# Kernel tuning notes

Measured on AMD Instinct MI355X. Metric: run time of the kernel, lower is better.

Reference implementation:

```python
import jax, jax.numpy as jnp
import numpy as np

B, C, H, W = 32, 512, 28, 28
NC, NM, K = 50, 4, 5          # num_classes, num_mixtures, num_clutter_models
OCC = 0.3                     # occ_likely[0]


def setup_inputs() -> dict:
    key = jax.random.key(0)
    k1, k2, k3 = jax.random.split(key, 3)
    x = jax.random.uniform(k1, (B, C, H, W), dtype=jnp.float32)
    mix_model = jax.random.uniform(k2, (NC * NM, C, H, W), dtype=jnp.float32)
    clutter_model = jax.random.uniform(k3, (K, C), dtype=jnp.float32)
    return {"x": x, "mix_model": mix_model, "clutter_model": clutter_model}


def _l1_normalize(a, axis):
    # torch: F.normalize(torch.clamp(a, 0, 1), p=1, dim=axis) with eps=1e-12
    a = jnp.clip(a, 0.0, 1.0)
    return a / jnp.maximum(jnp.sum(a, axis=axis, keepdims=True), 1e-12)


def reference(x, mix_model, clutter_model):
    # clutter: [K, C] -> L1-normalized over channels
    cl = _l1_normalize(clutter_model, axis=1)
    # background log-likelihood: (x.unsqueeze(1) * cl[:, :, None, None]).sum(2)
    bg = jnp.einsum('bchw,kc->bkhw', x, cl)            # [B, K, H, W]
    bg = jnp.log(bg * OCC + 1e-10)
    # mixture models: [M, C, H, W] -> L1-normalized over channels
    mm = _l1_normalize(mix_model, axis=1)
    # foreground log-likelihood: (x.unsqueeze(1) * mm).sum(2)
    fg = jnp.einsum('bchw,mchw->bmhw', x, mm)          # [B, M, H, W]
    fg = jnp.log(fg * (1.0 - OCC) + 1e-10)
    fg = fg.reshape(B, NC, NM, 1, H, W)
    # per-pixel occlusion max between foreground and background, sum over H, W
    per_model = jnp.maximum(fg, bg[:, None, None, :, :, :]).sum((-1, -2))  # [B, NC, NM, K]
    # max over clutter models, then over mixtures
    return per_model.max(axis=-1).max(axis=-1)          # [B, NC]
```

## Files before the change

### kernel.cpp

```cpp
#include <hip/hip_runtime.h>
#include <math.h>

#define Bc  32
#define Cc  512
#define HWc 784
#define Mc  200
#define Kc  5
#define NCc 50

#define PT    16
#define MT    32
#define CK    8
#define SPL   2
#define CSPL  256
#define NCH   32
#define NMT   7
#define NPT   49
#define CHF   4096

__device__ __forceinline__ void gl2lds16(const float* g, float* l) {
    __builtin_amdgcn_global_load_lds(
        (const __attribute__((address_space(1))) void*)g,
        (__attribute__((address_space(3))) void*)l, 16, 0, 0);
}

__global__ __launch_bounds__(256) void k_bg(const float* __restrict__ x,
                                            const float* __restrict__ clut,
                                            float* __restrict__ bgpart) {
    __shared__ float cl[Kc * Cc];
    __shared__ float csum[Kc];
    const int t = threadIdx.x;
    for (int i = t; i < Kc * Cc; i += 256) cl[i] = clut[i];
    __syncthreads();
    if (t < 160) {
        const int k = t >> 5, l = t & 31;
        float s = 0.0f;
        for (int c = l; c < Cc; c += 32) s += cl[k * Cc + c];
#pragma unroll
        for (int off = 16; off > 0; off >>= 1) s += __shfl_down(s, off, 32);
        if (l == 0) csum[k] = fmaxf(s, 1e-12f);
    }
    __syncthreads();

    const int b = blockIdx.x;
    const int z = blockIdx.z;
    const int hw = blockIdx.y * 256 + t;
    if (hw < HWc) {
        float acc[Kc] = {0.f, 0.f, 0.f, 0.f, 0.f};
        const int cbase = z * 128;
        const float* xb = x + ((size_t)b * Cc + cbase) * HWc + hw;
#pragma unroll 4
        for (int c = 0; c < 128; ++c) {
            const float xv = xb[c * HWc];
#pragma unroll
            for (int k = 0; k < Kc; ++k) acc[k] = fmaf(xv, cl[k * Cc + cbase + c], acc[k]);
        }
#pragma unroll
        for (int k = 0; k < Kc; ++k)
            bgpart[(((z * Bc + b) * Kc) + k) * HWc + hw] = acc[k] / csum[k];
    }
}

__global__ void k_bgsum(const float* __restrict__ bgpart, float* __restrict__ bgl) {
    const int i = blockIdx.x * 256 + threadIdx.x;
    const int N = Bc * Kc * HWc;
    if (i < N) {
        const float s = bgpart[i] + bgpart[i + N] + bgpart[i + 2 * N] + bgpart[i + 3 * N];
        bgl[i] = logf(0.3f * s + 1e-10f);
    }
}

__global__ __launch_bounds__(256) __attribute__((amdgpu_waves_per_eu(2, 2)))
void k_fg(const float* __restrict__ x, const float* __restrict__ mm,
          float* __restrict__ dotp, float* __restrict__ Sp) {
    __shared__ float ldsX[2][CHF];
    __shared__ float ldsM[2][CHF];

    const int t    = threadIdx.x;
    const int pixl = t & 3;
    const int mgr  = (t >> 2) & 3;
    const int bgp  = (t >> 4) & 3;
    const int pixh = t >> 6;
    const int pix  = pixl + 4 * pixh;

    const int mtile = blockIdx.x % NMT;
    const int ptile = (blockIdx.x / NMT) % NPT;
    const int split = blockIdx.x / (NMT * NPT);
    const int pix0  = ptile * PT;
    const int m0    = mtile * MT;
    const int c0    = split * CSPL;

    const int q4   = (t & 3) * 4;
    const int srow = (t >> 2) & 31;
    const int cx0  = t >> 7;
    const int mrow = (m0 + srow < Mc) ? (m0 + srow) : 0;
    const int ldst = 4 * t;

    int xg = (srow * Cc + c0 + cx0) * HWc + pix0 + q4;
    int mg = (mrow * Cc + c0 + cx0) * HWc + pix0 + q4;

    const int xoff = bgp * PT + pix;
    const int moff = mgr * PT + pix;

    float acc[8][8];
#pragma unroll
    for (int i = 0; i < 8; ++i)
#pragma unroll
        for (int j = 0; j < 8; ++j) acc[i][j] = 0.0f;
    float sacc[8] = {0.f, 0.f, 0.f, 0.f, 0.f, 0.f, 0.f, 0.f};

#pragma unroll
    for (int r = 0; r < 4; ++r) {
        gl2lds16(x + xg + 2 * r * HWc, &ldsX[0][ldst + 1024 * r]);
        gl2lds16(mm + mg + 2 * r * HWc, &ldsM[0][ldst + 1024 * r]);
    }
    xg += CK * HWc;
    mg += CK * HWc;

#pragma unroll 2
    for (int ch = 0; ch < NCH; ++ch) {
        __syncthreads();
        if (ch + 1 < NCH) {
            float* bx = &ldsX[(ch + 1) & 1][0];
            float* bm = &ldsM[(ch + 1) & 1][0];
#pragma unroll
            for (int r = 0; r < 4; ++r) {
                gl2lds16(x + xg + 2 * r * HWc, bx + ldst + 1024 * r);
                gl2lds16(mm + mg + 2 * r * HWc, bm + ldst + 1024 * r);
            }
            xg += CK * HWc;
            mg += CK * HWc;
        }
        const float* cbx = &ldsX[ch & 1][0];
        const float* cbm = &ldsM[ch & 1][0];
#pragma unroll
        for (int c = 0; c < CK; ++c) {
            float xv[8], mv[8];
#pragma unroll
            for (int i = 0; i < 8; ++i) xv[i] = cbx[c * 512 + 64 * i + xoff];
#pragma unroll
            for (int j = 0; j < 8; ++j) mv[j] = cbm[c * 512 + 64 * j + moff];
#pragma unroll
            for (int j = 0; j < 8; ++j) sacc[j] += mv[j];
#pragma unroll
            for (int i = 0; i < 8; ++i)
#pragma unroll
                for (int j = 0; j < 8; ++j)
                    acc[i][j] = fmaf(xv[i], mv[j], acc[i][j]);
        }
    }

    const int hw = pix0 + pix;
#pragma unroll
    for (int j = 0; j < 8; ++j) {
        const int m = m0 + mgr + 4 * j;
        if (m < Mc) {
            if (bgp == 0) Sp[(split * Mc + m) * HWc + hw] = sacc[j];
#pragma unroll
            for (int i = 0; i < 8; ++i) {
                const int b = bgp + 4 * i;
                dotp[((split * Mc + m) * Bc + b) * HWc + hw] = acc[i][j];
            }
        }
    }
}

__global__ __launch_bounds__(256) void k_red(const float* __restrict__ dotp,
                                             const float* __restrict__ Sp,
                                             const float* __restrict__ bgl,
                                             float* __restrict__ pm) {
    const int bm = blockIdx.x;
    const int b = bm / Mc;
    const int m = bm % Mc;
    const int t = threadIdx.x;
    const float* d0 = dotp + ((size_t)m * Bc + b) * HWc;
    const float* d1 = dotp + ((size_t)(Mc + m) * Bc + b) * HWc;
    const float* s0 = Sp + (size_t)m * HWc;
    const float* s1 = Sp + (size_t)(Mc + m) * HWc;
    const float* bgb = bgl + (size_t)b * Kc * HWc;

    float s[Kc] = {0.f, 0.f, 0.f, 0.f, 0.f};
    for (int hw = t; hw < HWc; hw += 256) {
        const float dot = d0[hw] + d1[hw];
        const float S   = s0[hw] + s1[hw];
        const float fgv = logf(0.7f * dot / fmaxf(S, 1e-12f) + 1e-10f);
#pragma unroll
        for (int k = 0; k < Kc; ++k) s[k] += fmaxf(fgv, bgb[k * HWc + hw]);
    }
#pragma unroll
    for (int off = 32; off > 0; off >>= 1) {
#pragma unroll
        for (int k = 0; k < Kc; ++k) s[k] += __shfl_down(s[k], off, 64);
    }
    __shared__ float red[4][Kc];
    const int wv = t >> 6, ln = t & 63;
    if (ln == 0) {
#pragma unroll
        for (int k = 0; k < Kc; ++k) red[wv][k] = s[k];
    }
    __syncthreads();
    if (t == 0) {
        float best = -INFINITY;
#pragma unroll
        for (int k = 0; k < Kc; ++k)
            best = fmaxf(best, red[0][k] + red[1][k] + red[2][k] + red[3][k]);
        pm[bm] = best;
    }
}

__global__ void k_out(const float* __restrict__ pm, float* __restrict__ out) {
    const int i = blockIdx.x * 256 + threadIdx.x;
    if (i < Bc * NCc) {
        const int b = i / NCc, nc = i % NCc;
        const float* p = pm + (size_t)b * Mc + nc * 4;
        out[i] = fmaxf(fmaxf(p[0], p[1]), fmaxf(p[2], p[3]));
    }
}

extern "C" void kernel_launch(void* const* d_in, const int* in_sizes, int n_in,
                              void* d_out, int out_size, void* d_ws, size_t ws_size,
                              hipStream_t stream) {
    const float* x    = (const float*)d_in[0];
    const float* mixm = (const float*)d_in[1];
    const float* clut = (const float*)d_in[2];
    float* out = (float*)d_out;

    float* dotp   = (float*)d_ws;
    float* Sp     = dotp + (size_t)SPL * Mc * Bc * HWc;
    float* bgpart = Sp + (size_t)SPL * Mc * HWc;
    float* bgl    = bgpart + (size_t)4 * Bc * Kc * HWc;
    float* pm     = bgl + (size_t)Bc * Kc * HWc;

    k_bg   <<<dim3(Bc, 4, 4), 256, 0, stream>>>(x, clut, bgpart);
    k_bgsum<<<dim3((Bc * Kc * HWc + 255) / 256), 256, 0, stream>>>(bgpart, bgl);
    k_fg   <<<dim3(NMT * NPT * SPL), 256, 0, stream>>>(x, mixm, dotp, Sp);
    k_red  <<<dim3(Bc * Mc), 256, 0, stream>>>(dotp, Sp, bgl, pm);
    k_out  <<<dim3(7), 256, 0, stream>>>(pm, out);
}
```

Measured before the change: 606.4 us.

## Compute foreground dot products with bf16 MFMA and fuse normalization and log

The fp32 FMA outer-product kernel is replaced by one that converts x and mixture tiles to bf16 in LDS and uses 16x16x32 bf16 MFMA instructions. A ones-vector MFMA produces the channel sums. The channel split is dropped, so the L1 normalization and log are applied directly in the epilogue and the reduce kernel reads a single fg array. This cuts FMA work and intermediate traffic, but bf16 rounding lowers precision and loads are now synchronous register-staged rather than async double-buffered.

```diff
diff --git a/kernel.cpp b/kernel.cpp
--- a/kernel.cpp
+++ b/kernel.cpp
@@ -8,20 +8,29 @@
 #define Kc  5
 #define NCc 50
 
-#define PT    16
-#define MT    32
-#define CK    8
-#define SPL   2
-#define CSPL  256
-#define NCH   32
-#define NMT   7
-#define NPT   49
-#define CHF   4096
-
-__device__ __forceinline__ void gl2lds16(const float* g, float* l) {
-    __builtin_amdgcn_global_load_lds(
-        (const __attribute__((address_space(1))) void*)g,
-        (__attribute__((address_space(3))) void*)l, 16, 0, 0);
+#define PTm   16
+#define MTm   16
+#define NMB   13
+#define NPB   49
+#define CKm   32
+#define NCHm  16
+#define RSTR  18
+#define XPL   (32*RSTR)
+#define MPL   (16*RSTR)
+#define MMBASE (16*XPL)
+#define LDSDW (16*XPL + 16*MPL)
+
+typedef short s8v __attribute__((ext_vector_type(8)));
+typedef float f4v __attribute__((ext_vector_type(4)));
+
+union F8 { uint2 u2[2]; s8v h; };
+
+__device__ __forceinline__ unsigned f2b(float f) {
+    union { float f; unsigned u; } v; v.f = f;
+    return (v.u + 0x7FFFu + ((v.u >> 16) & 1u)) >> 16;
+}
+__device__ __forceinline__ unsigned pk(float lo, float hi) {
+    return f2b(lo) | (f2b(hi) << 16);
 }
 
 __global__ __launch_bounds__(256) void k_bg(const float* __restrict__ x,
@@ -72,120 +81,143 @@
 
 __global__ __launch_bounds__(256) __attribute__((amdgpu_waves_per_eu(2, 2)))
 void k_fg(const float* __restrict__ x, const float* __restrict__ mm,
-          float* __restrict__ dotp, float* __restrict__ Sp) {
-    __shared__ float ldsX[2][CHF];
-    __shared__ float ldsM[2][CHF];
-
-    const int t    = threadIdx.x;
-    const int pixl = t & 3;
-    const int mgr  = (t >> 2) & 3;
-    const int bgp  = (t >> 4) & 3;
-    const int pixh = t >> 6;
-    const int pix  = pixl + 4 * pixh;
-
-    const int mtile = blockIdx.x % NMT;
-    const int ptile = (blockIdx.x / NMT) % NPT;
-    const int split = blockIdx.x / (NMT * NPT);
-    const int pix0  = ptile * PT;
-    const int m0    = mtile * MT;
-    const int c0    = split * CSPL;
-
-    const int q4   = (t & 3) * 4;
-    const int srow = (t >> 2) & 31;
-    const int cx0  = t >> 7;
-    const int mrow = (m0 + srow < Mc) ? (m0 + srow) : 0;
-    const int ldst = 4 * t;
-
-    int xg = (srow * Cc + c0 + cx0) * HWc + pix0 + q4;
-    int mg = (mrow * Cc + c0 + cx0) * HWc + pix0 + q4;
-
-    const int xoff = bgp * PT + pix;
-    const int moff = mgr * PT + pix;
-
-    float acc[8][8];
-#pragma unroll
-    for (int i = 0; i < 8; ++i)
-#pragma unroll
-        for (int j = 0; j < 8; ++j) acc[i][j] = 0.0f;
-    float sacc[8] = {0.f, 0.f, 0.f, 0.f, 0.f, 0.f, 0.f, 0.f};
-
-#pragma unroll
-    for (int r = 0; r < 4; ++r) {
-        gl2lds16(x + xg + 2 * r * HWc, &ldsX[0][ldst + 1024 * r]);
-        gl2lds16(mm + mg + 2 * r * HWc, &ldsM[0][ldst + 1024 * r]);
-    }
-    xg += CK * HWc;
-    mg += CK * HWc;
-
-#pragma unroll 2
-    for (int ch = 0; ch < NCH; ++ch) {
+          float* __restrict__ fg) {
+    __shared__ unsigned lds[LDSDW];
+
+    const int t = threadIdx.x;
+    const int mblk = blockIdx.x % NMB;
+    const int pix0 = (blockIdx.x / NMB) * PTm;
+
+    int xoff[4], xl[4];
+#pragma unroll
+    for (int g = 0; g < 4; ++g) {
+        const int G = t + 256 * g;
+        const int q = G & 3, b = (G >> 2) & 31, cg = G >> 7;
+        xoff[g] = (b * Cc + cg * 4) * HWc + pix0 + 4 * q;
+        xl[g]   = 4 * q * XPL + b * RSTR + cg * 2;
+    }
+    int moff[2], ml[2];
+    float mzero[2];
+#pragma unroll
+    for (int g = 0; g < 2; ++g) {
+        const int G = t + 256 * g;
+        const int q = G & 3, mr = (G >> 2) & 15, cg = (G >> 6) & 7;
+        const int mrow = mblk * MTm + mr;
+        mzero[g] = (mrow < Mc) ? 1.0f : 0.0f;
+        const int mc = (mrow < Mc) ? mrow : (Mc - 1);
+        moff[g] = (mc * Cc + cg * 4) * HWc + pix0 + 4 * q;
+        ml[g]   = MMBASE + 4 * q * MPL + mr * RSTR + cg * 2;
+    }
+
+    const int lane = t & 63;
+    const int w    = t >> 6;
+    const int row18q = (lane & 15) * RSTR + (lane >> 4) * 4;
+
+    f4v accD[4][2], accS[4];
+#pragma unroll
+    for (int p = 0; p < 4; ++p) {
+        accS[p] = (f4v)0.0f;
+#pragma unroll
+        for (int bt = 0; bt < 2; ++bt) accD[p][bt] = (f4v)0.0f;
+    }
+    const s8v ones = {0x3F80, 0x3F80, 0x3F80, 0x3F80, 0x3F80, 0x3F80, 0x3F80, 0x3F80};
+
+#pragma unroll 1
+    for (int ch = 0; ch < NCHm; ++ch) {
         __syncthreads();
-        if (ch + 1 < NCH) {
-            float* bx = &ldsX[(ch + 1) & 1][0];
-            float* bm = &ldsM[(ch + 1) & 1][0];
-#pragma unroll
-            for (int r = 0; r < 4; ++r) {
-                gl2lds16(x + xg + 2 * r * HWc, bx + ldst + 1024 * r);
-                gl2lds16(mm + mg + 2 * r * HWc, bm + ldst + 1024 * r);
-            }
-            xg += CK * HWc;
-            mg += CK * HWc;
-        }
-        const float* cbx = &ldsX[ch & 1][0];
-        const float* cbm = &ldsM[ch & 1][0];
-#pragma unroll
-        for (int c = 0; c < CK; ++c) {
-            float xv[8], mv[8];
-#pragma unroll
-            for (int i = 0; i < 8; ++i) xv[i] = cbx[c * 512 + 64 * i + xoff];
-#pragma unroll
-            for (int j = 0; j < 8; ++j) mv[j] = cbm[c * 512 + 64 * j + moff];
-#pragma unroll
-            for (int j = 0; j < 8; ++j) sacc[j] += mv[j];
-#pragma unroll
-            for (int i = 0; i < 8; ++i)
-#pragma unroll
-                for (int j = 0; j < 8; ++j)
-                    acc[i][j] = fmaf(xv[i], mv[j], acc[i][j]);
-        }
-    }
-
-    const int hw = pix0 + pix;
-#pragma unroll
-    for (int j = 0; j < 8; ++j) {
-        const int m = m0 + mgr + 4 * j;
-        if (m < Mc) {
-            if (bgp == 0) Sp[(split * Mc + m) * HWc + hw] = sacc[j];
-#pragma unroll
-            for (int i = 0; i < 8; ++i) {
-                const int b = bgp + 4 * i;
-                dotp[((split * Mc + m) * Bc + b) * HWc + hw] = acc[i][j];
-            }
-        }
-    }
-}
-
-__global__ __launch_bounds__(256) void k_red(const float* __restrict__ dotp,
-                                             const float* __restrict__ Sp,
+        float4 LX[4][4], LM[2][4];
+#pragma unroll
+        for (int g = 0; g < 4; ++g)
+#pragma unroll
+            for (int cc = 0; cc < 4; ++cc)
+                LX[g][cc] = *(const float4*)(x + xoff[g] + cc * HWc);
+#pragma unroll
+        for (int g = 0; g < 2; ++g)
+#pragma unroll
+            for (int cc = 0; cc < 4; ++cc)
+                LM[g][cc] = *(const float4*)(mm + moff[g] + cc * HWc);
+#pragma unroll
+        for (int g = 0; g < 4; ++g) xoff[g] += CKm * HWc;
+#pragma unroll
+        for (int g = 0; g < 2; ++g) moff[g] += CKm * HWc;
+
+#pragma unroll
+        for (int g = 0; g < 4; ++g) {
+            const float* f0 = (const float*)&LX[g][0];
+            const float* f1 = (const float*)&LX[g][1];
+            const float* f2 = (const float*)&LX[g][2];
+            const float* f3 = (const float*)&LX[g][3];
+#pragma unroll
+            for (int p = 0; p < 4; ++p)
+                *(uint2*)&lds[xl[g] + p * XPL] =
+                    make_uint2(pk(f0[p], f1[p]), pk(f2[p], f3[p]));
+        }
+#pragma unroll
+        for (int g = 0; g < 2; ++g) {
+            const float z = mzero[g];
+            const float* f0 = (const float*)&LM[g][0];
+            const float* f1 = (const float*)&LM[g][1];
+            const float* f2 = (const float*)&LM[g][2];
+            const float* f3 = (const float*)&LM[g][3];
+#pragma unroll
+            for (int p = 0; p < 4; ++p)
+                *(uint2*)&lds[ml[g] + p * MPL] =
+                    make_uint2(pk(f0[p] * z, f1[p] * z), pk(f2[p] * z, f3[p] * z));
+        }
+        __syncthreads();
+
+#pragma unroll
+        for (int p = 0; p < 4; ++p) {
+            const int pixg = w * 4 + p;
+            const unsigned* Xp = &lds[pixg * XPL + row18q];
+            const unsigned* Mp = &lds[MMBASE + pixg * MPL + row18q];
+            F8 a0, a1, bf;
+            a0.u2[0] = *(const uint2*)(Xp);
+            a0.u2[1] = *(const uint2*)(Xp + 2);
+            a1.u2[0] = *(const uint2*)(Xp + 16 * RSTR);
+            a1.u2[1] = *(const uint2*)(Xp + 16 * RSTR + 2);
+            bf.u2[0] = *(const uint2*)(Mp);
+            bf.u2[1] = *(const uint2*)(Mp + 2);
+            accD[p][0] = __builtin_amdgcn_mfma_f32_16x16x32_bf16(a0.h, bf.h, accD[p][0], 0, 0, 0);
+            accD[p][1] = __builtin_amdgcn_mfma_f32_16x16x32_bf16(a1.h, bf.h, accD[p][1], 0, 0, 0);
+            accS[p]    = __builtin_amdgcn_mfma_f32_16x16x32_bf16(ones, bf.h, accS[p],    0, 0, 0);
+        }
+    }
+
+    const int m = mblk * MTm + (lane & 15);
+    if (m < Mc) {
+        const int quad = lane >> 4;
+#pragma unroll
+        for (int p = 0; p < 4; ++p) {
+            const int hw = pix0 + w * 4 + p;
+            const float scale = 0.7f / fmaxf(accS[p][0], 1e-12f);
+#pragma unroll
+            for (int bt = 0; bt < 2; ++bt)
+#pragma unroll
+                for (int r = 0; r < 4; ++r) {
+                    const int b = bt * 16 + quad * 4 + r;
+                    fg[((size_t)m * Bc + b) * HWc + hw] =
+                        logf(accD[p][bt][r] * scale + 1e-10f);
+                }
+        }
+    }
+}
+
+__global__ __launch_bounds__(256) void k_red(const float* __restrict__ fg,
                                              const float* __restrict__ bgl,
                                              float* __restrict__ pm) {
     const int bm = blockIdx.x;
     const int b = bm / Mc;
     const int m = bm % Mc;
     const int t = threadIdx.x;
-    const float* d0 = dotp + ((size_t)m * Bc + b) * HWc;
-    const float* d1 = dotp + ((size_t)(Mc + m) * Bc + b) * HWc;
-    const float* s0 = Sp + (size_t)m * HWc;
-    const float* s1 = Sp + (size_t)(Mc + m) * HWc;
+    const float* fgp = fg + ((size_t)m * Bc + b) * HWc;
     const float* bgb = bgl + (size_t)b * Kc * HWc;
 
     float s[Kc] = {0.f, 0.f, 0.f, 0.f, 0.f};
     for (int hw = t; hw < HWc; hw += 256) {
-        const float dot = d0[hw] + d1[hw];
-        const float S   = s0[hw] + s1[hw];
-        const float fgv = logf(0.7f * dot / fmaxf(S, 1e-12f) + 1e-10f);
-#pragma unroll
-        for (int k = 0; k < Kc; ++k) s[k] += fmaxf(fgv, bgb[k * HWc + hw]);
+        const float f = fgp[hw];
+#pragma unroll
+        for (int k = 0; k < Kc; ++k) s[k] += fmaxf(f, bgb[k * HWc + hw]);
     }
 #pragma unroll
     for (int off = 32; off > 0; off >>= 1) {
@@ -225,15 +257,14 @@
     const float* clut = (const float*)d_in[2];
     float* out = (float*)d_out;
 
-    float* dotp   = (float*)d_ws;
-    float* Sp     = dotp + (size_t)SPL * Mc * Bc * HWc;
-    float* bgpart = Sp + (size_t)SPL * Mc * HWc;
+    float* fg     = (float*)d_ws;
+    float* bgpart = fg + (size_t)Mc * Bc * HWc;
     float* bgl    = bgpart + (size_t)4 * Bc * Kc * HWc;
     float* pm     = bgl + (size_t)Bc * Kc * HWc;
 
     k_bg   <<<dim3(Bc, 4, 4), 256, 0, stream>>>(x, clut, bgpart);
     k_bgsum<<<dim3((Bc * Kc * HWc + 255) / 256), 256, 0, stream>>>(bgpart, bgl);
-    k_fg   <<<dim3(NMT * NPT * SPL), 256, 0, stream>>>(x, mixm, dotp, Sp);
-    k_red  <<<dim3(Bc * Mc), 256, 0, stream>>>(dotp, Sp, bgl, pm);
+    k_fg   <<<dim3(NMB * NPB), 256, 0, stream>>>(x, mixm, fg);
+    k_red  <<<dim3(Bc * Mc), 256, 0, stream>>>(fg, bgl, pm);
     k_out  <<<dim3(7), 256, 0, stream>>>(pm, out);
 }
```

Result: faster. 577.2 us (-4.8%).
